# Kernel tuning notes

Hardware: AMD Instinct MI355X
Metric: run time of the kernel (lower is better)

Reference implementation:

```python
import jax, jax.numpy as jnp
import numpy as np

INNER_DIM = 512
SCALE = 1.0 / np.sqrt(INNER_DIM).astype(np.float32)  # module scales by 1/sqrt(inner_dim), not head_dim


def setup_inputs() -> dict:
    key = jax.random.key(0)
    ks = jax.random.split(key, 7)
    b, n, d = 4, 4096, 512
    s = 0.02
    return {
        "x": jax.random.normal(ks[0], (b, n, d), jnp.float32),
        "y": jax.random.normal(ks[1], (b, n, d), jnp.float32),
        "Wq": jax.random.normal(ks[2], (INNER_DIM, d), jnp.float32) * s,  # torch Linear weight [out, in]
        "Wk": jax.random.normal(ks[3], (INNER_DIM, d), jnp.float32) * s,
        "Wv": jax.random.normal(ks[4], (INNER_DIM, d), jnp.float32) * s,
        "Wo": jax.random.normal(ks[5], (d, INNER_DIM), jnp.float32) * s,
        "bo": jax.random.normal(ks[6], (d,), jnp.float32) * s,
    }


def reference(x, y, Wq, Wk, Wv, Wo, bo):
    # q, k from x; v from y (bias-free projections)
    q = jnp.einsum('bnd,id->bni', x, Wq)
    k = jnp.einsum('bnd,id->bni', x, Wk)
    v = jnp.einsum('bnd,id->bni', y, Wv)
    # full [b, n, n] scores, scaled by 1/sqrt(inner_dim)
    alpha = jnp.einsum('bik,bjk->bij', q, k) * SCALE
    alpha = jax.nn.softmax(alpha, axis=-1)
    ctx = jnp.einsum('bij,bjd->bid', alpha, v)
    out = jnp.einsum('bid,od->bio', ctx, Wo) + bo
    return out
```

## Files before the change

### kernel.cpp

```cpp
#include <hip/hip_runtime.h>
#include <hip/hip_bf16.h>


typedef unsigned short u16;
typedef __bf16 bf16x8 __attribute__((ext_vector_type(8)));
typedef float f32x4 __attribute__((ext_vector_type(4)));

#define SCALE_QK 0.044194173824159216f

__device__ __forceinline__ u16 f2bf(float f) {
    __hip_bfloat16 h = __float2bfloat16(f);
    return __builtin_bit_cast(u16, h);
}

__device__ __forceinline__ void load_lds16(const void* g, void* l) {
    __builtin_amdgcn_global_load_lds(
        (const __attribute__((address_space(1))) void*)g,
        (__attribute__((address_space(3))) void*)l, 16, 0, 0);
}

__global__ void cvt_bf16_kernel(const float* __restrict__ src, u16* __restrict__ dst,
                                int n8, float scale) {
    int i = blockIdx.x * blockDim.x + threadIdx.x;
    if (i >= n8) return;
    const float4* s4 = (const float4*)src;
    float4 v0 = s4[2 * i], v1 = s4[2 * i + 1];
    union { u16 u[8]; uint4 v; } o;
    o.u[0] = f2bf(v0.x * scale); o.u[1] = f2bf(v0.y * scale);
    o.u[2] = f2bf(v0.z * scale); o.u[3] = f2bf(v0.w * scale);
    o.u[4] = f2bf(v1.x * scale); o.u[5] = f2bf(v1.y * scale);
    o.u[6] = f2bf(v1.z * scale); o.u[7] = f2bf(v1.w * scale);
    ((uint4*)dst)[i] = o.v;
}

__global__ void wvo_kernel(const float* __restrict__ Wo, const float* __restrict__ Wv,
                           float* __restrict__ Wvo) {
    int ob = blockIdx.x * 4, t = threadIdx.x;
    float a[4][2] = {{0.f, 0.f}, {0.f, 0.f}, {0.f, 0.f}, {0.f, 0.f}};
    for (int i = 0; i < 512; ++i) {
        float v0 = Wv[i * 512 + t], v1 = Wv[i * 512 + t + 256];
#pragma unroll
        for (int r = 0; r < 4; ++r) {
            float w = Wo[(ob + r) * 512 + i];
            a[r][0] += w * v0;
            a[r][1] += w * v1;
        }
    }
#pragma unroll
    for (int r = 0; r < 4; ++r) {
        Wvo[(ob + r) * 512 + t] = a[r][0];
        Wvo[(ob + r) * 512 + t + 256] = a[r][1];
    }
}

__launch_bounds__(512, 2)
__global__ void gemm256_exp_kernel(const u16* __restrict__ A, const u16* __restrict__ B,
                                   u16* __restrict__ Cout, int N, int lda, int ldb,
                                   long long sAz, long long sBz, long long sCz) {
    __shared__ u16 lds[8][8192];

    const int tid = threadIdx.x;
    const int wave = tid >> 6, lane = tid & 63;
    const int lr = lane & 15, lg = lane >> 4;
    const int wm = wave >> 2, wn = wave & 3;

    int bid = (blockIdx.z * gridDim.y + blockIdx.y) * gridDim.x + blockIdx.x;
    int lgc = (bid & 7) * 128 + (bid >> 3);
    const int bx = lgc & 15;
    int rem = lgc >> 4;
    const int by = rem & 15, z = rem >> 4;
    const int row0 = by * 256, col0 = bx * 256;

    const u16* Ab = A + (size_t)z * sAz;
    const u16* Bb = B + (size_t)z * sBz;

    const int rb = lane >> 2;
    const int kg8 = ((lane & 3) ^ (rb & 3)) << 3;

    f32x4 acc[8][4];
#pragma unroll
    for (int i = 0; i < 8; ++i)
#pragma unroll
        for (int j = 0; j < 4; ++j) acc[i][j] = (f32x4){0.f, 0.f, 0.f, 0.f};

#define STAGE_HALF(s_, slot_)                                                     \
    {                                                                             \
        const int h_ = (s_)&3, ts_ = (s_) >> 2;                                   \
        const u16* G_ = (h_ & 1) ? Bb : Ab;                                       \
        const int pan_ = (h_ & 1) ? col0 : row0;                                  \
        const int ld_ = (h_ & 1) ? ldb : lda;                                     \
        const int kofs_ = ts_ * 64 + (h_ >> 1) * 32 + kg8;                        \
        _Pragma("unroll") for (int j_ = 0; j_ < 2; ++j_) {                        \
            int r_ = (j_ * 8 + wave) * 16 + rb;                                   \
            load_lds16(G_ + (size_t)(pan_ + r_) * ld_ + kofs_,                    \
                       &lds[slot_][(j_ * 8 + wave) * 512]);                       \
        }                                                                         \
    }

    #pragma unroll
    for (int s = 0; s < 6; ++s) STAGE_HALF(s, s);
    asm volatile("s_waitcnt vmcnt(4)");
    __builtin_amdgcn_sched_barrier(0);
    __builtin_amdgcn_s_barrier();

    bf16x8 bfr[4];

#pragma unroll
    for (int i = 0; i < 4; ++i) {
#pragma unroll
        for (int p = 0; p < 8; ++p) {
            const int q = p & 3;
            const int ks = q >> 1;
            const int aslot = (p >> 2) * 4 + 2 * ks;
            const int bslot = aslot + 1;
            const int fmb = (q & 1) * 4;

            bf16x8 af[4];
#pragma unroll
            for (int f = 0; f < 4; ++f) {
                int row = wm * 128 + (fmb + f) * 16 + lr;
                af[f] = *(const bf16x8*)&lds[aslot][row * 32 + ((lg ^ (lr & 3)) << 3)];
            }
            if (q == 0 || q == 2) {
#pragma unroll
                for (int f = 0; f < 4; ++f) {
                    int row = wn * 64 + f * 16 + lr;
                    bfr[f] = *(const bf16x8*)&lds[bslot][row * 32 + ((lg ^ (lr & 3)) << 3)];
                }
            }

            {
                const int s = 8 * i + p + 6;
                if (s < 32) {
                    const int slot = (p + 6) & 7;
                    STAGE_HALF(s, slot);
                }
            }

            __builtin_amdgcn_sched_barrier(0);
            __builtin_amdgcn_s_barrier();
            asm volatile("s_waitcnt lgkmcnt(0)");
            __builtin_amdgcn_sched_barrier(0);

            __builtin_amdgcn_s_setprio(1);
#pragma unroll
            for (int f = 0; f < 4; ++f)
#pragma unroll
                for (int n = 0; n < 4; ++n)
                    acc[fmb + f][n] = __builtin_amdgcn_mfma_f32_16x16x32_bf16(
                        af[f], bfr[n], acc[fmb + f][n], 0, 0, 0);
            __builtin_amdgcn_s_setprio(0);

            if (p == 3) {
                if (i == 3) asm volatile("s_waitcnt vmcnt(0)");
                else        asm volatile("s_waitcnt vmcnt(4)");
            } else if (p == 7 && i < 3) {
                asm volatile("s_waitcnt vmcnt(4)");
            }
            __builtin_amdgcn_sched_barrier(0);
            __builtin_amdgcn_s_barrier();
        }
    }
#undef STAGE_HALF

    u16* C = Cout + (size_t)z * sCz;
#pragma unroll
    for (int fm = 0; fm < 8; ++fm)
#pragma unroll
        for (int fn = 0; fn < 4; ++fn)
#pragma unroll
            for (int reg = 0; reg < 4; ++reg) {
                int r = row0 + wm * 128 + fm * 16 + lg * 4 + reg;
                int c = col0 + wn * 64 + fn * 16 + lr;
                C[(size_t)r * N + c] = f2bf(__expf(acc[fm][fn][reg]));
            }
}

__launch_bounds__(512, 2)
__global__ void pv8_kernel(const u16* __restrict__ P, const u16* __restrict__ vwT,
                           float* __restrict__ part, float* __restrict__ lpart) {
    __shared__ u16 lds[8][8192];

    const int tid = threadIdx.x;
    const int wave = tid >> 6, lane = tid & 63;
    const int lr = lane & 15, lg = lane >> 4;
    const int wm = wave >> 2, wn = wave & 3;

    int bid = blockIdx.x;
    int lgc = (bid & 7) * 32 + (bid >> 3);
    const int rp = lgc & 15;
    const int t5 = lgc >> 4;
    const int cx = t5 & 1, ks = (t5 >> 1) & 1, z = t5 >> 2;
    const int row0 = rp * 256;
    const int col0 = cx * 256;

    const u16* Ab = P + (size_t)z * 16777216 + (size_t)ks * 2048;
    const u16* Bb = vwT + (size_t)z * 2097152 + (size_t)ks * 2048;

    const int rb = lane >> 2;
    const int kg8 = ((lane & 3) ^ (rb & 3)) << 3;

    f32x4 acc[8][4];
#pragma unroll
    for (int i = 0; i < 8; ++i)
#pragma unroll
        for (int j = 0; j < 4; ++j) acc[i][j] = (f32x4){0.f, 0.f, 0.f, 0.f};
    float rsm[8] = {0.f, 0.f, 0.f, 0.f, 0.f, 0.f, 0.f, 0.f};

#define STAGE_HALF(s_, slot_)                                                     \
    {                                                                             \
        const int h_ = (s_)&3, ts_ = (s_) >> 2;                                   \
        const u16* G_ = (h_ & 1) ? Bb : Ab;                                       \
        const int pan_ = (h_ & 1) ? col0 : row0;                                  \
        const int kofs_ = ts_ * 64 + (h_ >> 1) * 32 + kg8;                        \
        _Pragma("unroll") for (int j_ = 0; j_ < 2; ++j_) {                        \
            int r_ = (j_ * 8 + wave) * 16 + rb;                                   \
            load_lds16(G_ + (size_t)(pan_ + r_) * 4096 + kofs_,                   \
                       &lds[slot_][(j_ * 8 + wave) * 512]);                       \
        }                                                                         \
    }

    #pragma unroll
    for (int s = 0; s < 6; ++s) STAGE_HALF(s, s);
    asm volatile("s_waitcnt vmcnt(4)");
    __builtin_amdgcn_sched_barrier(0);
    __builtin_amdgcn_s_barrier();

    bf16x8 bfr[4];

    for (int i = 0; i < 16; ++i) {
#pragma unroll
        for (int p = 0; p < 8; ++p) {
            const int q = p & 3;
            const int ksl = q >> 1;
            const int aslot = (p >> 2) * 4 + 2 * ksl;
            const int bslot = aslot + 1;
            const int fmb = (q & 1) * 4;

            bf16x8 af[4];
#pragma unroll
            for (int f = 0; f < 4; ++f) {
                int row = wm * 128 + (fmb + f) * 16 + lr;
                af[f] = *(const bf16x8*)&lds[aslot][row * 32 + ((lg ^ (lr & 3)) << 3)];
            }
            if (q == 0 || q == 2) {
#pragma unroll
                for (int f = 0; f < 4; ++f) {
                    int row = wn * 64 + f * 16 + lr;
                    bfr[f] = *(const bf16x8*)&lds[bslot][row * 32 + ((lg ^ (lr & 3)) << 3)];
                }
            }

            {
                const int s = 8 * i + p + 6;
                if (s < 128) {
                    const int slot = (p + 6) & 7;
                    STAGE_HALF(s, slot);
                }
            }

            __builtin_amdgcn_sched_barrier(0);
            __builtin_amdgcn_s_barrier();
            asm volatile("s_waitcnt lgkmcnt(0)");
            __builtin_amdgcn_sched_barrier(0);

            __builtin_amdgcn_s_setprio(1);
#pragma unroll
            for (int f = 0; f < 4; ++f)
#pragma unroll
                for (int n = 0; n < 4; ++n)
                    acc[fmb + f][n] = __builtin_amdgcn_mfma_f32_16x16x32_bf16(
                        af[f], bfr[n], acc[fmb + f][n], 0, 0, 0);
            __builtin_amdgcn_s_setprio(0);

            if (wn == 0) {
#pragma unroll
                for (int f = 0; f < 4; ++f) {
                    union { bf16x8 v; unsigned u[4]; } cv;
                    cv.v = af[f];
#pragma unroll
                    for (int w = 0; w < 4; ++w)
                        rsm[fmb + f] += __uint_as_float(cv.u[w] << 16) +
                                        __uint_as_float(cv.u[w] & 0xffff0000u);
                }
            }

            if (p == 3) {
                if (i == 15) asm volatile("s_waitcnt vmcnt(0)");
                else         asm volatile("s_waitcnt vmcnt(4)");
            } else if (p == 7 && i < 15) {
                asm volatile("s_waitcnt vmcnt(4)");
            }
            __builtin_amdgcn_sched_barrier(0);
            __builtin_amdgcn_s_barrier();
        }
    }
#undef STAGE_HALF

    if (wn == 0) {
#pragma unroll
        for (int j = 0; j < 8; ++j) {
            rsm[j] += __shfl_xor(rsm[j], 16, 64);
            rsm[j] += __shfl_xor(rsm[j], 32, 64);
        }
        if (cx == 0 && lg == 0) {
            float* lp = lpart + (size_t)ks * 16384 + z * 4096 + row0 + wm * 128;
#pragma unroll
            for (int j = 0; j < 8; ++j) lp[j * 16 + lr] = rsm[j];
        }
    }

    float* O = part + (size_t)ks * 8388608 + ((size_t)z * 4096 + row0) * 512;
#pragma unroll
    for (int fm = 0; fm < 8; ++fm)
#pragma unroll
        for (int fn = 0; fn < 4; ++fn) {
            int c = col0 + wn * 64 + fn * 16 + lr;
#pragma unroll
            for (int reg = 0; reg < 4; ++reg) {
                int r = wm * 128 + fm * 16 + lg * 4 + reg;
                O[(size_t)r * 512 + c] = acc[fm][fn][reg];
            }
        }
}

template <int EPI>
__launch_bounds__(256)
__global__ void gemm_f32a_kernel(const float* __restrict__ A, const u16* __restrict__ B,
                                 void* __restrict__ Cout, int N, int K, int lda, int ldb) {
    __shared__ u16 As[2][128 * 32];
    __shared__ u16 Bs[2][128 * 32];

    const int tid = threadIdx.x;
    const int wave = tid >> 6, lane = tid & 63;
    const int lr = lane & 15, lg = lane >> 4;
    const int wr = wave >> 1, wc = wave & 1;

    const int gx = gridDim.x, gy = gridDim.y;
    int bid = blockIdx.y * gx + blockIdx.x;
    const int nwg = gx * gy;
    int lgc = (bid & 7) * (nwg >> 3) + (bid >> 3);
    const int bx = lgc % gx, by = lgc / gx;
    const int row0 = by * 128, col0 = bx * 128;

    f32x4 acc[4][4];
#pragma unroll
    for (int i = 0; i < 4; ++i)
#pragma unroll
        for (int j = 0; j < 4; ++j) acc[i][j] = (f32x4){0.f, 0.f, 0.f, 0.f};

    const int KT = K >> 5;
    float4 ar[2][2];

#define LOADA(kt2)                                                                \
    {                                                                             \
        _Pragma("unroll") for (int i = 0; i < 2; ++i) {                           \
            int chunk = i * 256 + tid;                                            \
            int r = chunk >> 2, c4 = chunk & 3;                                   \
            const float* src = A + (size_t)(row0 + r) * lda + (kt2) * 32 + c4 * 8;\
            ar[i][0] = *(const float4*)src;                                       \
            ar[i][1] = *(const float4*)(src + 4);                                 \
        }                                                                         \
    }
#define WRITEA(bufi)                                                              \
    {                                                                             \
        _Pragma("unroll") for (int i = 0; i < 2; ++i) {                           \
            int chunk = i * 256 + tid;                                            \
            union { u16 u[8]; uint4 v; } cv;                                      \
            const float* f = (const float*)&ar[i][0];                             \
            _Pragma("unroll") for (int j = 0; j < 8; ++j) cv.u[j] = f2bf(f[j]);   \
            *(uint4*)&As[bufi][chunk * 8] = cv.v;                                 \
        }                                                                         \
    }
#define STAGEB(bufi, kt2)                                                         \
    {                                                                             \
        _Pragma("unroll") for (int i = 0; i < 2; ++i) {                           \
            int chunk = i * 256 + tid;                                            \
            int r = chunk >> 2, c4 = chunk & 3;                                   \
            load_lds16(B + (size_t)(col0 + r) * ldb + (kt2) * 32 + c4 * 8,        \
                       &Bs[bufi][(i * 256 + wave * 64) * 8]);                     \
        }                                                                         \
    }

    LOADA(0);
    WRITEA(0);
    LOADA(1);
    STAGEB(0, 0);
    int buf = 0;
    for (int kt = 0; kt < KT; ++kt) {
        __syncthreads();
        if (kt + 1 < KT) {
            WRITEA(buf ^ 1);
            STAGEB(buf ^ 1, kt + 1);
        }
        if (kt + 2 < KT) LOADA(kt + 2);

        bf16x8 af[4], bfr[4];
#pragma unroll
        for (int mf = 0; mf < 4; ++mf)
            af[mf] = *(const bf16x8*)&As[buf][(wr * 64 + mf * 16 + lr) * 32 + lg * 8];
#pragma unroll
        for (int nf = 0; nf < 4; ++nf)
            bfr[nf] = *(const bf16x8*)&Bs[buf][(wc * 64 + nf * 16 + lr) * 32 + lg * 8];
#pragma unroll
        for (int mf = 0; mf < 4; ++mf)
#pragma unroll
            for (int nf = 0; nf < 4; ++nf)
                acc[mf][nf] = __builtin_amdgcn_mfma_f32_16x16x32_bf16(
                    af[mf], bfr[nf], acc[mf][nf], 0, 0, 0);
        buf ^= 1;
    }
#undef LOADA
#undef WRITEA
#undef STAGEB

    const int rbase = row0 + wr * 64;
    const int cbase = col0 + wc * 64;

    if (EPI == 0) {
        u16* C = (u16*)Cout;
#pragma unroll
        for (int mf = 0; mf < 4; ++mf)
#pragma unroll
            for (int nf = 0; nf < 4; ++nf)
#pragma unroll
                for (int reg = 0; reg < 4; ++reg) {
                    int r = rbase + mf * 16 + lg * 4 + reg;
                    int c = cbase + nf * 16 + lr;
                    C[(size_t)r * N + c] = f2bf(acc[mf][nf][reg]);
                }
    } else {
        u16* C = (u16*)Cout;
#pragma unroll
        for (int mf = 0; mf < 4; ++mf)
#pragma unroll
            for (int nf = 0; nf < 4; ++nf) {
                int rg = rbase + mf * 16 + lg * 4;
                int bsel = rg >> 12, rl = rg & 4095;
                int c = cbase + nf * 16 + lr;
                union { u16 u[4]; uint2 v; } o;
#pragma unroll
                for (int reg = 0; reg < 4; ++reg) o.u[reg] = f2bf(acc[mf][nf][reg]);
                *(uint2*)(C + ((size_t)bsel << 21) + ((size_t)c << 12) + rl) = o.v;
            }
    }
}

__global__ void reduce_kernel(const float* __restrict__ part,
                              const float* __restrict__ lpart,
                              const float* __restrict__ bo,
                              float* __restrict__ out) {
    int i = blockIdx.x * blockDim.x + threadIdx.x;
    int r = i >> 7, c4 = i & 127;
    float inv = 1.0f / (lpart[r] + lpart[16384 + r]);
    float4 a = ((const float4*)part)[i];
    float4 b = ((const float4*)part)[i + 2097152];
    float4 bi = ((const float4*)bo)[c4];
    float4 o;
    o.x = (a.x + b.x) * inv + bi.x;
    o.y = (a.y + b.y) * inv + bi.y;
    o.z = (a.z + b.z) * inv + bi.z;
    o.w = (a.w + b.w) * inv + bi.w;
    ((float4*)out)[i] = o;
}

extern "C" void kernel_launch(void* const* d_in, const int* in_sizes, int n_in,
                              void* d_out, int out_size, void* d_ws, size_t ws_size,
                              hipStream_t stream) {
    const float* x  = (const float*)d_in[0];
    const float* y  = (const float*)d_in[1];
    const float* Wq = (const float*)d_in[2];
    const float* Wk = (const float*)d_in[3];
    const float* Wv = (const float*)d_in[4];
    const float* Wo = (const float*)d_in[5];
    const float* bo = (const float*)d_in[6];
    float* out = (float*)d_out;

    char* ws = (char*)d_ws;
    u16*   qk   = (u16*)(ws + 0);
    float* part = (float*)(ws + 0);
    u16*   vwT  = (u16*)(ws + 67108864);
    u16*   Wqkb = (u16*)(ws + 83886080);
    u16*   Wvob = (u16*)(ws + 84934656);
    float* Wvo  = (float*)(ws + 85458944);
    float* lpart= (float*)(ws + 86507520);
    u16*   P    = (u16*)(ws + 86638592);

    cvt_bf16_kernel<<<128, 256, 0, stream>>>(Wq, Wqkb, 32768, SCALE_QK);
    cvt_bf16_kernel<<<128, 256, 0, stream>>>(Wk, Wqkb + 262144, 32768, 1.0f);
    wvo_kernel<<<128, 256, 0, stream>>>(Wo, Wv, Wvo);
    cvt_bf16_kernel<<<128, 256, 0, stream>>>(Wvo, Wvob, 32768, 1.0f);

    gemm_f32a_kernel<0><<<dim3(8, 128), 256, 0, stream>>>(x, Wqkb, qk, 1024, 512, 512, 512);
    gemm_f32a_kernel<1><<<dim3(4, 128), 256, 0, stream>>>(y, Wvob, vwT, 512, 512, 512, 512);

    gemm256_exp_kernel<<<dim3(16, 16, 4), 512, 0, stream>>>(qk, qk + 512, P,
                                                            4096, 1024, 1024,
                                                            4194304, 4194304, 16777216);

    pv8_kernel<<<256, 512, 0, stream>>>(P, vwT, part, lpart);

    reduce_kernel<<<8192, 256, 0, stream>>>(part, lpart, bo, out);
}
```

Measured before the change: 334.2 us.

## Pre-convert activations to bf16 and change LDS swizzle in attention GEMMs

Adds standalone kernels that convert x and y to bf16 up front, so the projection GEMM can stage both operands with direct global-to-LDS loads instead of loading fp32 into registers and converting them in the loop. The generalized GEMM also gains batch strides. Separately, the LDS XOR swizzle in the QK-exp and PV kernels now keys on row bits 1-2 instead of 0-1, to cut bank conflicts on fragment reads. The cost is two extra conversion passes over the activations and more workspace traffic.

```diff
diff --git a/kernel.cpp b/kernel.cpp
--- a/kernel.cpp
+++ b/kernel.cpp
@@ -63,6 +63,7 @@
     const int wave = tid >> 6, lane = tid & 63;
     const int lr = lane & 15, lg = lane >> 4;
     const int wm = wave >> 2, wn = wave & 3;
+    const int rsw = (lg ^ ((lr >> 1) & 3)) << 3;
 
     int bid = (blockIdx.z * gridDim.y + blockIdx.y) * gridDim.x + blockIdx.x;
     int lgc = (bid & 7) * 128 + (bid >> 3);
@@ -75,7 +76,7 @@
     const u16* Bb = B + (size_t)z * sBz;
 
     const int rb = lane >> 2;
-    const int kg8 = ((lane & 3) ^ (rb & 3)) << 3;
+    const int kg8 = ((lane & 3) ^ ((rb >> 1) & 3)) << 3;
 
     f32x4 acc[8][4];
 #pragma unroll
@@ -119,13 +120,13 @@
 #pragma unroll
             for (int f = 0; f < 4; ++f) {
                 int row = wm * 128 + (fmb + f) * 16 + lr;
-                af[f] = *(const bf16x8*)&lds[aslot][row * 32 + ((lg ^ (lr & 3)) << 3)];
+                af[f] = *(const bf16x8*)&lds[aslot][row * 32 + rsw];
             }
             if (q == 0 || q == 2) {
 #pragma unroll
                 for (int f = 0; f < 4; ++f) {
                     int row = wn * 64 + f * 16 + lr;
-                    bfr[f] = *(const bf16x8*)&lds[bslot][row * 32 + ((lg ^ (lr & 3)) << 3)];
+                    bfr[f] = *(const bf16x8*)&lds[bslot][row * 32 + rsw];
                 }
             }
 
@@ -185,6 +186,7 @@
     const int wave = tid >> 6, lane = tid & 63;
     const int lr = lane & 15, lg = lane >> 4;
     const int wm = wave >> 2, wn = wave & 3;
+    const int rsw = (lg ^ ((lr >> 1) & 3)) << 3;
 
     int bid = blockIdx.x;
     int lgc = (bid & 7) * 32 + (bid >> 3);
@@ -198,7 +200,7 @@
     const u16* Bb = vwT + (size_t)z * 2097152 + (size_t)ks * 2048;
 
     const int rb = lane >> 2;
-    const int kg8 = ((lane & 3) ^ (rb & 3)) << 3;
+    const int kg8 = ((lane & 3) ^ ((rb >> 1) & 3)) << 3;
 
     f32x4 acc[8][4];
 #pragma unroll
@@ -241,13 +243,13 @@
 #pragma unroll
             for (int f = 0; f < 4; ++f) {
                 int row = wm * 128 + (fmb + f) * 16 + lr;
-                af[f] = *(const bf16x8*)&lds[aslot][row * 32 + ((lg ^ (lr & 3)) << 3)];
+                af[f] = *(const bf16x8*)&lds[aslot][row * 32 + rsw];
             }
             if (q == 0 || q == 2) {
 #pragma unroll
                 for (int f = 0; f < 4; ++f) {
                     int row = wn * 64 + f * 16 + lr;
-                    bfr[f] = *(const bf16x8*)&lds[bslot][row * 32 + ((lg ^ (lr & 3)) << 3)];
+                    bfr[f] = *(const bf16x8*)&lds[bslot][row * 32 + rsw];
                 }
             }
 
@@ -326,8 +328,9 @@
 
 template <int EPI>
 __launch_bounds__(256)
-__global__ void gemm_f32a_kernel(const float* __restrict__ A, const u16* __restrict__ B,
-                                 void* __restrict__ Cout, int N, int K, int lda, int ldb) {
+__global__ void gemm_bt_kernel(const u16* __restrict__ A, const u16* __restrict__ B,
+                               void* __restrict__ Cout, int N, int K, int lda, int ldb,
+                               long long sAz, long long sBz, long long sCz) {
     __shared__ u16 As[2][128 * 32];
     __shared__ u16 Bs[2][128 * 32];
 
@@ -337,12 +340,17 @@
     const int wr = wave >> 1, wc = wave & 1;
 
     const int gx = gridDim.x, gy = gridDim.y;
-    int bid = blockIdx.y * gx + blockIdx.x;
-    const int nwg = gx * gy;
+    int bid = (blockIdx.z * gy + blockIdx.y) * gx + blockIdx.x;
+    const int nwg = gx * gy * gridDim.z;
     int lgc = (bid & 7) * (nwg >> 3) + (bid >> 3);
-    const int bx = lgc % gx, by = lgc / gx;
+    const int bx = lgc % gx;
+    int rem = lgc / gx;
+    const int by = rem % gy, z = rem / gy;
     const int row0 = by * 128, col0 = bx * 128;
 
+    const u16* Ab = A + (size_t)z * sAz;
+    const u16* Bb = B + (size_t)z * sBz;
+
     f32x4 acc[4][4];
 #pragma unroll
     for (int i = 0; i < 4; ++i)
@@ -350,50 +358,24 @@
         for (int j = 0; j < 4; ++j) acc[i][j] = (f32x4){0.f, 0.f, 0.f, 0.f};
 
     const int KT = K >> 5;
-    float4 ar[2][2];
-
-#define LOADA(kt2)                                                                \
+
+#define STAGE(bufi, kt2)                                                          \
     {                                                                             \
         _Pragma("unroll") for (int i = 0; i < 2; ++i) {                           \
             int chunk = i * 256 + tid;                                            \
             int r = chunk >> 2, c4 = chunk & 3;                                   \
-            const float* src = A + (size_t)(row0 + r) * lda + (kt2) * 32 + c4 * 8;\
-            ar[i][0] = *(const float4*)src;                                       \
-            ar[i][1] = *(const float4*)(src + 4);                                 \
-        }                                                                         \
-    }
-#define WRITEA(bufi)                                                              \
-    {                                                                             \
-        _Pragma("unroll") for (int i = 0; i < 2; ++i) {                           \
-            int chunk = i * 256 + tid;                                            \
-            union { u16 u[8]; uint4 v; } cv;                                      \
-            const float* f = (const float*)&ar[i][0];                             \
-            _Pragma("unroll") for (int j = 0; j < 8; ++j) cv.u[j] = f2bf(f[j]);   \
-            *(uint4*)&As[bufi][chunk * 8] = cv.v;                                 \
-        }                                                                         \
-    }
-#define STAGEB(bufi, kt2)                                                         \
-    {                                                                             \
-        _Pragma("unroll") for (int i = 0; i < 2; ++i) {                           \
-            int chunk = i * 256 + tid;                                            \
-            int r = chunk >> 2, c4 = chunk & 3;                                   \
-            load_lds16(B + (size_t)(col0 + r) * ldb + (kt2) * 32 + c4 * 8,        \
+            load_lds16(Ab + (size_t)(row0 + r) * lda + (kt2) * 32 + c4 * 8,       \
+                       &As[bufi][(i * 256 + wave * 64) * 8]);                     \
+            load_lds16(Bb + (size_t)(col0 + r) * ldb + (kt2) * 32 + c4 * 8,       \
                        &Bs[bufi][(i * 256 + wave * 64) * 8]);                     \
         }                                                                         \
     }
 
-    LOADA(0);
-    WRITEA(0);
-    LOADA(1);
-    STAGEB(0, 0);
+    STAGE(0, 0);
     int buf = 0;
     for (int kt = 0; kt < KT; ++kt) {
         __syncthreads();
-        if (kt + 1 < KT) {
-            WRITEA(buf ^ 1);
-            STAGEB(buf ^ 1, kt + 1);
-        }
-        if (kt + 2 < KT) LOADA(kt + 2);
+        if (kt + 1 < KT) STAGE(buf ^ 1, kt + 1);
 
         bf16x8 af[4], bfr[4];
 #pragma unroll
@@ -410,15 +392,13 @@
                     af[mf], bfr[nf], acc[mf][nf], 0, 0, 0);
         buf ^= 1;
     }
-#undef LOADA
-#undef WRITEA
-#undef STAGEB
+#undef STAGE
 
     const int rbase = row0 + wr * 64;
     const int cbase = col0 + wc * 64;
 
     if (EPI == 0) {
-        u16* C = (u16*)Cout;
+        u16* C = (u16*)Cout + (size_t)z * sCz;
 #pragma unroll
         for (int mf = 0; mf < 4; ++mf)
 #pragma unroll
@@ -477,7 +457,9 @@
     float* out = (float*)d_out;
 
     char* ws = (char*)d_ws;
-    u16*   qk   = (u16*)(ws + 0);
+    u16*   xb   = (u16*)(ws + 0);
+    u16*   yb   = (u16*)(ws + 16777216);
+    u16*   qk   = (u16*)(ws + 33554432);
     float* part = (float*)(ws + 0);
     u16*   vwT  = (u16*)(ws + 67108864);
     u16*   Wqkb = (u16*)(ws + 83886080);
@@ -486,13 +468,18 @@
     float* lpart= (float*)(ws + 86507520);
     u16*   P    = (u16*)(ws + 86638592);
 
+    cvt_bf16_kernel<<<4096, 256, 0, stream>>>(x, xb, 1048576, 1.0f);
+    cvt_bf16_kernel<<<4096, 256, 0, stream>>>(y, yb, 1048576, 1.0f);
     cvt_bf16_kernel<<<128, 256, 0, stream>>>(Wq, Wqkb, 32768, SCALE_QK);
     cvt_bf16_kernel<<<128, 256, 0, stream>>>(Wk, Wqkb + 262144, 32768, 1.0f);
+
     wvo_kernel<<<128, 256, 0, stream>>>(Wo, Wv, Wvo);
     cvt_bf16_kernel<<<128, 256, 0, stream>>>(Wvo, Wvob, 32768, 1.0f);
 
-    gemm_f32a_kernel<0><<<dim3(8, 128), 256, 0, stream>>>(x, Wqkb, qk, 1024, 512, 512, 512);
-    gemm_f32a_kernel<1><<<dim3(4, 128), 256, 0, stream>>>(y, Wvob, vwT, 512, 512, 512, 512);
+    gemm_bt_kernel<0><<<dim3(8, 128, 1), 256, 0, stream>>>(xb, Wqkb, qk,
+                                                           1024, 512, 512, 512, 0, 0, 0);
+    gemm_bt_kernel<1><<<dim3(4, 128, 1), 256, 0, stream>>>(yb, Wvob, vwT,
+                                                           512, 512, 512, 512, 0, 0, 0);
 
     gemm256_exp_kernel<<<dim3(16, 16, 4), 512, 0, stream>>>(qk, qk + 512, P,
                                                             4096, 1024, 1024,
```

Measured after the change: 330.6 us. About the same (-1.1%).
